# Kernel tuning notes

Hardware: AMD Instinct MI355X
Metric: run time of the kernel (lower is better)

Reference implementation:

```python
import jax, jax.numpy as jnp
import numpy as np

NUM_STEPS = 8
SLOPE = 25.0        # snntorch surrogate.fast_sigmoid default slope
MAX_STD = 2.0
MIN_STD = 0.1
STATE_DIM = 6
HIDDEN = 128
OUT = 1
BATCH = 65536
W_STD = 0.01


@jax.custom_vjp
def spike(x):
    # heaviside(x) with fast-sigmoid surrogate gradient
    return (x > 0).astype(x.dtype)

def _spike_fwd(x):
    return spike(x), x

def _spike_bwd(x, g):
    return (g / (SLOPE * jnp.abs(x) + 1.0) ** 2,)

spike.defvjp(_spike_fwd, _spike_bwd)


def setup_inputs() -> dict:
    key = jax.random.key(0)
    ks = jax.random.split(key, 8)
    state = jax.random.normal(ks[0], (BATCH, STATE_DIM), dtype=jnp.float32)
    w_fc1 = W_STD * jax.random.normal(ks[1], (HIDDEN, STATE_DIM), dtype=jnp.float32)
    w_rec1 = W_STD * jax.random.normal(ks[2], (HIDDEN, HIDDEN), dtype=jnp.float32)
    w_fc2 = W_STD * jax.random.normal(ks[3], (HIDDEN, HIDDEN), dtype=jnp.float32)
    w_rec2 = W_STD * jax.random.normal(ks[4], (HIDDEN, HIDDEN), dtype=jnp.float32)
    w_mean = W_STD * jax.random.normal(ks[5], (OUT, HIDDEN), dtype=jnp.float32)
    w_std = W_STD * jax.random.normal(ks[6], (OUT, HIDDEN), dtype=jnp.float32)
    return {
        "state": state,
        "w_fc1": w_fc1, "w_rec1": w_rec1,
        "w_fc2": w_fc2, "w_rec2": w_rec2,
        "w_mean": w_mean, "w_std": w_std,
        "alpha1": jnp.float32(0.9), "beta1": jnp.float32(0.9), "thr1": jnp.float32(1.0),
        "alpha2": jnp.float32(0.9), "beta2": jnp.float32(0.9), "thr2": jnp.float32(1.0),
    }


def _snn_forward(state, w_fc1, w_rec1, w_fc2, w_rec2, w_mean, w_std,
                 alpha1, beta1, thr1, alpha2, beta2, thr2):
    a1 = jnp.clip(alpha1, 0.0, 1.0); b1 = jnp.clip(beta1, 0.0, 1.0)
    a2 = jnp.clip(alpha2, 0.0, 1.0); b2 = jnp.clip(beta2, 0.0, 1.0)

    B = state.shape[0]
    cur1_in = state @ w_fc1.T  # constant across steps: [B, H]
    z = jnp.zeros((B, HIDDEN), dtype=state.dtype)

    def step(carry, _):
        syn1, mem1, spk1, syn2, mem2, spk2 = carry
        # layer 1: snntorch Synaptic (reset-by-subtract, reset from prev mem, detached)
        reset1 = jax.lax.stop_gradient((mem1 - thr1 > 0).astype(mem1.dtype))
        syn1 = a1 * syn1 + cur1_in + spk1 @ w_rec1.T
        mem1 = b1 * mem1 + syn1 - reset1 * thr1
        spk1 = spike(mem1 - thr1)
        # layer 2
        reset2 = jax.lax.stop_gradient((mem2 - thr2 > 0).astype(mem2.dtype))
        syn2 = a2 * syn2 + spk1 @ w_fc2.T + spk2 @ w_rec2.T
        mem2 = b2 * mem2 + syn2 - reset2 * thr2
        spk2 = spike(mem2 - thr2)
        return (syn1, mem1, spk1, syn2, mem2, spk2), spk2

    init = (z, z, z, z, z, z)
    _, spk_rec = jax.lax.scan(step, init, None, length=NUM_STEPS)  # [T, B, H]
    avg_spikes = spk_rec.mean(axis=0)  # [B, H]

    value_mean = jnp.tanh(avg_spikes @ w_mean.T)
    value_std = (MAX_STD - MIN_STD) * jax.nn.sigmoid(avg_spikes @ w_std.T + 2.0) + MIN_STD
    return value_mean, value_std


def reference(state, w_fc1, w_rec1, w_fc2, w_rec2, w_mean, w_std,
              alpha1, beta1, thr1, alpha2, beta2, thr2):
    return _snn_forward(state, w_fc1, w_rec1, w_fc2, w_rec2, w_mean, w_std,
                        alpha1, beta1, thr1, alpha2, beta2, thr2)
```

## Files before the change

kernel.cpp:

```cpp
#include <hip/hip_runtime.h>
#include <cmath>


constexpr int BATCH = 65536;
constexpr int HID   = 128;
constexpr int SDIM  = 6;
constexpr int NSTEP = 8;
constexpr int BLOCK = 1024;
constexpr int GRID  = 256;
constexpr int WAVES_TOTAL = GRID * (BLOCK / 64);
constexpr int ELEMS_PER_WAVE = BATCH / WAVES_TOTAL;

__global__ __launch_bounds__(BLOCK) void snn_fwd(
    const float* __restrict__ state,
    const float* __restrict__ w_fc1,
    const float* __restrict__ w_rec1,
    const float* __restrict__ w_fc2,
    const float* __restrict__ w_rec2,
    const float* __restrict__ w_mean,
    const float* __restrict__ w_std,
    const float* __restrict__ p_alpha1, const float* __restrict__ p_beta1,
    const float* __restrict__ p_thr1,
    const float* __restrict__ p_alpha2, const float* __restrict__ p_beta2,
    const float* __restrict__ p_thr2,
    float* __restrict__ out)
{
    __shared__ float2 ld_rec1[HID * 64];
    __shared__ float2 ld_fc2 [HID * 64];
    __shared__ float2 ld_fc1 [SDIM * 64];
    __shared__ float  ld_wm[HID];
    __shared__ float  ld_wsd[HID];

    const int tid = threadIdx.x;

    for (int v = tid; v < HID * 64; v += BLOCK) {
        const int l = v >> 7;
        const int j = v & 127;
        const int pos = (j << 6) | (l ^ (j & 63));
        ld_rec1[pos] = make_float2(w_rec1[l * HID + j], w_rec1[(l + 64) * HID + j]);
        ld_fc2 [pos] = make_float2(w_fc2 [l * HID + j], w_fc2 [(l + 64) * HID + j]);
    }
    for (int v = tid; v < SDIM * 64; v += BLOCK) {
        const int k = v >> 6, l = v & 63;
        ld_fc1[(k << 6) | l] = make_float2(w_fc1[l * SDIM + k], w_fc1[(l + 64) * SDIM + k]);
    }
    if (tid < HID)               ld_wm [tid]        = w_mean[tid];
    else if (tid < 2 * HID)      ld_wsd[tid - HID]  = w_std [tid - HID];

    const float a1 = fminf(fmaxf(p_alpha1[0], 0.f), 1.f);
    const float b1 = fminf(fmaxf(p_beta1 [0], 0.f), 1.f);
    const float a2 = fminf(fmaxf(p_alpha2[0], 0.f), 1.f);
    const float b2 = fminf(fmaxf(p_beta2 [0], 0.f), 1.f);
    const float t1 = p_thr1[0];
    const float t2 = p_thr2[0];

    __syncthreads();

    const int lane  = tid & 63;
    const int gwave = blockIdx.x * (BLOCK / 64) + (tid >> 6);

    for (int e = 0; e < ELEMS_PER_WAVE; ++e) {
        const int b = gwave + WAVES_TOTAL * e;

        float cur_a = 0.f, cur_b = 0.f;
        #pragma unroll
        for (int k = 0; k < SDIM; ++k) {
            const float s = state[b * SDIM + k];
            const float2 w = ld_fc1[(k << 6) | lane];
            cur_a = fmaf(s, w.x, cur_a);
            cur_b = fmaf(s, w.y, cur_b);
        }

        float syn1a = 0.f, syn1b = 0.f, mem1a = 0.f, mem1b = 0.f;
        float syn2a = 0.f, syn2b = 0.f, mem2a = 0.f, mem2b = 0.f;
        bool  spk1a = false, spk1b = false, spk2a = false, spk2b = false;
        float cnt_a = 0.f, cnt_b = 0.f;
        unsigned long long m1a = 0ull, m1b = 0ull, m2a = 0ull, m2b = 0ull;

        #pragma unroll 1
        for (int t = 0; t < NSTEP; ++t) {
            float r_a = 0.f, r_b = 0.f;
            unsigned long long m = m1a;
            while (m) {
                const int j = __builtin_ctzll(m); m &= m - 1;
                const float2 w = ld_rec1[(j << 6) | (lane ^ j)];
                r_a += w.x; r_b += w.y;
            }
            m = m1b;
            while (m) {
                const int j0 = __builtin_ctzll(m); m &= m - 1;
                const int j = j0 + 64;
                const float2 w = ld_rec1[(j << 6) | (lane ^ j0)];
                r_a += w.x; r_b += w.y;
            }
            syn1a = fmaf(a1, syn1a, cur_a + r_a);
            syn1b = fmaf(a1, syn1b, cur_b + r_b);
            mem1a = fmaf(b1, mem1a, syn1a) - (spk1a ? t1 : 0.f);
            mem1b = fmaf(b1, mem1b, syn1b) - (spk1b ? t1 : 0.f);
            spk1a = (mem1a - t1) > 0.f;
            spk1b = (mem1b - t1) > 0.f;
            m1a = __ballot(spk1a);
            m1b = __ballot(spk1b);

            float f_a = 0.f, f_b = 0.f;
            m = m1a;
            while (m) {
                const int j = __builtin_ctzll(m); m &= m - 1;
                const float2 w = ld_fc2[(j << 6) | (lane ^ j)];
                f_a += w.x; f_b += w.y;
            }
            m = m1b;
            while (m) {
                const int j0 = __builtin_ctzll(m); m &= m - 1;
                const int j = j0 + 64;
                const float2 w = ld_fc2[(j << 6) | (lane ^ j0)];
                f_a += w.x; f_b += w.y;
            }
            m = m2a;
            while (m) {
                const int j = __builtin_ctzll(m); m &= m - 1;
                f_a += w_rec2[lane * HID + j];
                f_b += w_rec2[(lane + 64) * HID + j];
            }
            m = m2b;
            while (m) {
                const int j = __builtin_ctzll(m) + 64; m &= m - 1;
                f_a += w_rec2[lane * HID + j];
                f_b += w_rec2[(lane + 64) * HID + j];
            }
            syn2a = fmaf(a2, syn2a, f_a);
            syn2b = fmaf(a2, syn2b, f_b);
            mem2a = fmaf(b2, mem2a, syn2a) - (spk2a ? t2 : 0.f);
            mem2b = fmaf(b2, mem2b, syn2b) - (spk2b ? t2 : 0.f);
            spk2a = (mem2a - t2) > 0.f;
            spk2b = (mem2b - t2) > 0.f;
            m2a = __ballot(spk2a);
            m2b = __ballot(spk2b);
            cnt_a += spk2a ? 1.f : 0.f;
            cnt_b += spk2b ? 1.f : 0.f;
        }

        const float avg_a = cnt_a * (1.f / (float)NSTEP);
        const float avg_b = cnt_b * (1.f / (float)NSTEP);
        float dm = avg_a * ld_wm [lane] + avg_b * ld_wm [lane + 64];
        float ds = avg_a * ld_wsd[lane] + avg_b * ld_wsd[lane + 64];
        #pragma unroll
        for (int off = 32; off > 0; off >>= 1) {
            dm += __shfl_xor(dm, off, 64);
            ds += __shfl_xor(ds, off, 64);
        }
        if (lane == 0) {
            out[b]         = tanhf(dm);
            const float sg = 1.f / (1.f + expf(-(ds + 2.f)));
            out[BATCH + b] = 1.9f * sg + 0.1f;
        }
    }
}

extern "C" void kernel_launch(void* const* d_in, const int* in_sizes, int n_in,
                              void* d_out, int out_size, void* d_ws, size_t ws_size,
                              hipStream_t stream) {
    (void)in_sizes; (void)n_in; (void)d_ws; (void)ws_size; (void)out_size;
    snn_fwd<<<GRID, BLOCK, 0, stream>>>(
        (const float*)d_in[0],
        (const float*)d_in[1],
        (const float*)d_in[2],
        (const float*)d_in[3],
        (const float*)d_in[4],
        (const float*)d_in[5],
        (const float*)d_in[6],
        (const float*)d_in[7],
        (const float*)d_in[8],
        (const float*)d_in[9],
        (const float*)d_in[10],
        (const float*)d_in[11],
        (const float*)d_in[12],
        (float*)d_out);
}
```

Measured before the change: 129.8 us.

## Fuse rec1/fc2 spike gathers into one float4 table and interleave two batch elements

Packs w_rec1 and w_fc2 columns into a single float4 shared-memory table, so one LDS read per active layer-1 spike serves both the next step's recurrent sum and the current fc2 sum. The recurrent layer-1 sum is deferred to the next step, so the two sparse loops over layer-1 spikes become one. Each wave now processes two batch elements at once inside a shared while-loop, to expose more independent loads and raise ILP. The cost is higher register pressure, a wider LDS access per iteration, and branch divergence when the two elements have different spike counts.

```diff
diff --git a/kernel.cpp b/kernel.cpp
--- a/kernel.cpp
+++ b/kernel.cpp
@@ -25,9 +25,8 @@
     const float* __restrict__ p_thr2,
     float* __restrict__ out)
 {
-    __shared__ float2 ld_rec1[HID * 64];
-    __shared__ float2 ld_fc2 [HID * 64];
-    __shared__ float2 ld_fc1 [SDIM * 64];
+    __shared__ float4 ld_w [HID * 64];
+    __shared__ float2 ld_fc1[SDIM * 64];
     __shared__ float  ld_wm[HID];
     __shared__ float  ld_wsd[HID];
 
@@ -37,15 +36,15 @@
         const int l = v >> 7;
         const int j = v & 127;
         const int pos = (j << 6) | (l ^ (j & 63));
-        ld_rec1[pos] = make_float2(w_rec1[l * HID + j], w_rec1[(l + 64) * HID + j]);
-        ld_fc2 [pos] = make_float2(w_fc2 [l * HID + j], w_fc2 [(l + 64) * HID + j]);
+        ld_w[pos] = make_float4(w_rec1[l * HID + j], w_rec1[(l + 64) * HID + j],
+                                w_fc2 [l * HID + j], w_fc2 [(l + 64) * HID + j]);
     }
     for (int v = tid; v < SDIM * 64; v += BLOCK) {
         const int k = v >> 6, l = v & 63;
         ld_fc1[(k << 6) | l] = make_float2(w_fc1[l * SDIM + k], w_fc1[(l + 64) * SDIM + k]);
     }
-    if (tid < HID)               ld_wm [tid]        = w_mean[tid];
-    else if (tid < 2 * HID)      ld_wsd[tid - HID]  = w_std [tid - HID];
+    if (tid < HID)               ld_wm [tid]       = w_mean[tid];
+    else if (tid < 2 * HID)      ld_wsd[tid - HID] = w_std [tid - HID];
 
     const float a1 = fminf(fmaxf(p_alpha1[0], 0.f), 1.f);
     const float b1 = fminf(fmaxf(p_beta1 [0], 0.f), 1.f);
@@ -59,100 +58,128 @@
     const int lane  = tid & 63;
     const int gwave = blockIdx.x * (BLOCK / 64) + (tid >> 6);
 
-    for (int e = 0; e < ELEMS_PER_WAVE; ++e) {
-        const int b = gwave + WAVES_TOTAL * e;
-
-        float cur_a = 0.f, cur_b = 0.f;
+    for (int e = 0; e < ELEMS_PER_WAVE / 2; ++e) {
+        int bidx[2];
+        bidx[0] = gwave + WAVES_TOTAL * (2 * e);
+        bidx[1] = gwave + WAVES_TOTAL * (2 * e + 1);
+
+        float cur_a[2], cur_b[2];
+        float s1a[2] = {0.f, 0.f}, s1b[2] = {0.f, 0.f};
+        float m1a[2] = {0.f, 0.f}, m1b[2] = {0.f, 0.f};
+        float s2a[2] = {0.f, 0.f}, s2b[2] = {0.f, 0.f};
+        float m2a[2] = {0.f, 0.f}, m2b[2] = {0.f, 0.f};
+        float ra [2] = {0.f, 0.f}, rb [2] = {0.f, 0.f};
+        float cna[2] = {0.f, 0.f}, cnb[2] = {0.f, 0.f};
+        bool sp1a[2] = {false, false}, sp1b[2] = {false, false};
+        bool sp2a[2] = {false, false}, sp2b[2] = {false, false};
+        unsigned long long M2a[2] = {0ull, 0ull}, M2b[2] = {0ull, 0ull};
+
         #pragma unroll
-        for (int k = 0; k < SDIM; ++k) {
-            const float s = state[b * SDIM + k];
-            const float2 w = ld_fc1[(k << 6) | lane];
-            cur_a = fmaf(s, w.x, cur_a);
-            cur_b = fmaf(s, w.y, cur_b);
-        }
-
-        float syn1a = 0.f, syn1b = 0.f, mem1a = 0.f, mem1b = 0.f;
-        float syn2a = 0.f, syn2b = 0.f, mem2a = 0.f, mem2b = 0.f;
-        bool  spk1a = false, spk1b = false, spk2a = false, spk2b = false;
-        float cnt_a = 0.f, cnt_b = 0.f;
-        unsigned long long m1a = 0ull, m1b = 0ull, m2a = 0ull, m2b = 0ull;
+        for (int p = 0; p < 2; ++p) {
+            float ca = 0.f, cb = 0.f;
+            #pragma unroll
+            for (int k = 0; k < SDIM; ++k) {
+                const float s = state[bidx[p] * SDIM + k];
+                const float2 w = ld_fc1[(k << 6) | lane];
+                ca = fmaf(s, w.x, ca);
+                cb = fmaf(s, w.y, cb);
+            }
+            cur_a[p] = ca; cur_b[p] = cb;
+        }
 
         #pragma unroll 1
         for (int t = 0; t < NSTEP; ++t) {
-            float r_a = 0.f, r_b = 0.f;
-            unsigned long long m = m1a;
-            while (m) {
-                const int j = __builtin_ctzll(m); m &= m - 1;
-                const float2 w = ld_rec1[(j << 6) | (lane ^ j)];
-                r_a += w.x; r_b += w.y;
-            }
-            m = m1b;
-            while (m) {
-                const int j0 = __builtin_ctzll(m); m &= m - 1;
-                const int j = j0 + 64;
-                const float2 w = ld_rec1[(j << 6) | (lane ^ j0)];
-                r_a += w.x; r_b += w.y;
-            }
-            syn1a = fmaf(a1, syn1a, cur_a + r_a);
-            syn1b = fmaf(a1, syn1b, cur_b + r_b);
-            mem1a = fmaf(b1, mem1a, syn1a) - (spk1a ? t1 : 0.f);
-            mem1b = fmaf(b1, mem1b, syn1b) - (spk1b ? t1 : 0.f);
-            spk1a = (mem1a - t1) > 0.f;
-            spk1b = (mem1b - t1) > 0.f;
-            m1a = __ballot(spk1a);
-            m1b = __ballot(spk1b);
-
-            float f_a = 0.f, f_b = 0.f;
-            m = m1a;
-            while (m) {
-                const int j = __builtin_ctzll(m); m &= m - 1;
-                const float2 w = ld_fc2[(j << 6) | (lane ^ j)];
-                f_a += w.x; f_b += w.y;
-            }
-            m = m1b;
-            while (m) {
-                const int j0 = __builtin_ctzll(m); m &= m - 1;
-                const int j = j0 + 64;
-                const float2 w = ld_fc2[(j << 6) | (lane ^ j0)];
-                f_a += w.x; f_b += w.y;
-            }
-            m = m2a;
-            while (m) {
-                const int j = __builtin_ctzll(m); m &= m - 1;
-                f_a += w_rec2[lane * HID + j];
-                f_b += w_rec2[(lane + 64) * HID + j];
-            }
-            m = m2b;
-            while (m) {
-                const int j = __builtin_ctzll(m) + 64; m &= m - 1;
-                f_a += w_rec2[lane * HID + j];
-                f_b += w_rec2[(lane + 64) * HID + j];
-            }
-            syn2a = fmaf(a2, syn2a, f_a);
-            syn2b = fmaf(a2, syn2b, f_b);
-            mem2a = fmaf(b2, mem2a, syn2a) - (spk2a ? t2 : 0.f);
-            mem2b = fmaf(b2, mem2b, syn2b) - (spk2b ? t2 : 0.f);
-            spk2a = (mem2a - t2) > 0.f;
-            spk2b = (mem2b - t2) > 0.f;
-            m2a = __ballot(spk2a);
-            m2b = __ballot(spk2b);
-            cnt_a += spk2a ? 1.f : 0.f;
-            cnt_b += spk2b ? 1.f : 0.f;
-        }
-
-        const float avg_a = cnt_a * (1.f / (float)NSTEP);
-        const float avg_b = cnt_b * (1.f / (float)NSTEP);
-        float dm = avg_a * ld_wm [lane] + avg_b * ld_wm [lane + 64];
-        float ds = avg_a * ld_wsd[lane] + avg_b * ld_wsd[lane + 64];
+            unsigned long long u0, v0, u1, v1;
+            #pragma unroll
+            for (int p = 0; p < 2; ++p) {
+                s1a[p] = fmaf(a1, s1a[p], cur_a[p] + ra[p]);
+                s1b[p] = fmaf(a1, s1b[p], cur_b[p] + rb[p]);
+                m1a[p] = fmaf(b1, m1a[p], s1a[p]) - (sp1a[p] ? t1 : 0.f);
+                m1b[p] = fmaf(b1, m1b[p], s1b[p]) - (sp1b[p] ? t1 : 0.f);
+                sp1a[p] = (m1a[p] - t1) > 0.f;
+                sp1b[p] = (m1b[p] - t1) > 0.f;
+                ra[p] = 0.f; rb[p] = 0.f;
+            }
+            u0 = __ballot(sp1a[0]); v0 = __ballot(sp1b[0]);
+            u1 = __ballot(sp1a[1]); v1 = __ballot(sp1b[1]);
+
+            float fa[2] = {0.f, 0.f}, fb[2] = {0.f, 0.f};
+            while (u0 | v0 | u1 | v1) {
+                if (u0) {
+                    const int j = __builtin_ctzll(u0); u0 &= u0 - 1;
+                    const float4 w = ld_w[(j << 6) | (lane ^ j)];
+                    ra[0] += w.x; rb[0] += w.y; fa[0] += w.z; fb[0] += w.w;
+                }
+                if (v0) {
+                    const int j0 = __builtin_ctzll(v0); v0 &= v0 - 1;
+                    const float4 w = ld_w[((j0 + 64) << 6) | (lane ^ j0)];
+                    ra[0] += w.x; rb[0] += w.y; fa[0] += w.z; fb[0] += w.w;
+                }
+                if (u1) {
+                    const int j = __builtin_ctzll(u1); u1 &= u1 - 1;
+                    const float4 w = ld_w[(j << 6) | (lane ^ j)];
+                    ra[1] += w.x; rb[1] += w.y; fa[1] += w.z; fb[1] += w.w;
+                }
+                if (v1) {
+                    const int j0 = __builtin_ctzll(v1); v1 &= v1 - 1;
+                    const float4 w = ld_w[((j0 + 64) << 6) | (lane ^ j0)];
+                    ra[1] += w.x; rb[1] += w.y; fa[1] += w.z; fb[1] += w.w;
+                }
+            }
+
+            #pragma unroll
+            for (int p = 0; p < 2; ++p) {
+                unsigned long long m = M2a[p];
+                while (m) {
+                    const int j = __builtin_ctzll(m); m &= m - 1;
+                    fa[p] += w_rec2[lane * HID + j];
+                    fb[p] += w_rec2[(lane + 64) * HID + j];
+                }
+                m = M2b[p];
+                while (m) {
+                    const int j = __builtin_ctzll(m) + 64; m &= m - 1;
+                    fa[p] += w_rec2[lane * HID + j];
+                    fb[p] += w_rec2[(lane + 64) * HID + j];
+                }
+            }
+
+            #pragma unroll
+            for (int p = 0; p < 2; ++p) {
+                s2a[p] = fmaf(a2, s2a[p], fa[p]);
+                s2b[p] = fmaf(a2, s2b[p], fb[p]);
+                m2a[p] = fmaf(b2, m2a[p], s2a[p]) - (sp2a[p] ? t2 : 0.f);
+                m2b[p] = fmaf(b2, m2b[p], s2b[p]) - (sp2b[p] ? t2 : 0.f);
+                sp2a[p] = (m2a[p] - t2) > 0.f;
+                sp2b[p] = (m2b[p] - t2) > 0.f;
+                cna[p] += sp2a[p] ? 1.f : 0.f;
+                cnb[p] += sp2b[p] ? 1.f : 0.f;
+            }
+            M2a[0] = __ballot(sp2a[0]); M2b[0] = __ballot(sp2b[0]);
+            M2a[1] = __ballot(sp2a[1]); M2b[1] = __ballot(sp2b[1]);
+        }
+
+        float dm[2], ds[2];
+        #pragma unroll
+        for (int p = 0; p < 2; ++p) {
+            const float avg_a = cna[p] * (1.f / (float)NSTEP);
+            const float avg_b = cnb[p] * (1.f / (float)NSTEP);
+            dm[p] = avg_a * ld_wm [lane] + avg_b * ld_wm [lane + 64];
+            ds[p] = avg_a * ld_wsd[lane] + avg_b * ld_wsd[lane + 64];
+        }
         #pragma unroll
         for (int off = 32; off > 0; off >>= 1) {
-            dm += __shfl_xor(dm, off, 64);
-            ds += __shfl_xor(ds, off, 64);
+            dm[0] += __shfl_xor(dm[0], off, 64);
+            ds[0] += __shfl_xor(ds[0], off, 64);
+            dm[1] += __shfl_xor(dm[1], off, 64);
+            ds[1] += __shfl_xor(ds[1], off, 64);
         }
         if (lane == 0) {
-            out[b]         = tanhf(dm);
-            const float sg = 1.f / (1.f + expf(-(ds + 2.f)));
-            out[BATCH + b] = 1.9f * sg + 0.1f;
+            #pragma unroll
+            for (int p = 0; p < 2; ++p) {
+                out[bidx[p]] = tanhf(dm[p]);
+                const float sg = 1.f / (1.f + expf(-(ds[p] + 2.f)));
+                out[BATCH + bidx[p]] = 1.9f * sg + 0.1f;
+            }
         }
     }
 }
```

Result: slower. 132.8 us (+2.3%).

## Split SNN forward into separate layer-1 and layer-2 kernels via spike-mask workspace

Applied to the files above, without the earlier changes.

Splits the fused two-layer recurrence into two kernels that communicate through per-element spike bitmasks written to the workspace. Each kernel stages only one 64KB weight matrix in LDS, which allows more blocks per CU, and the grid is doubled. Layer 2 skips leading timesteps with no layer-1 spikes and skips the output reduction when no layer-2 neuron fired. It also drops the XOR swizzle on LDS indexing. In exchange it adds a second launch and a global round trip for the masks, and the unswizzled layout may bring back LDS bank conflicts.

```diff
diff --git a/kernel.cpp b/kernel.cpp
--- a/kernel.cpp
+++ b/kernel.cpp
@@ -1,66 +1,48 @@
 #include <hip/hip_runtime.h>
 #include <cmath>
 
+
+typedef unsigned long long u64;
 
 constexpr int BATCH = 65536;
 constexpr int HID   = 128;
 constexpr int SDIM  = 6;
 constexpr int NSTEP = 8;
 constexpr int BLOCK = 1024;
-constexpr int GRID  = 256;
+constexpr int GRID  = 512;
 constexpr int WAVES_TOTAL = GRID * (BLOCK / 64);
-constexpr int ELEMS_PER_WAVE = BATCH / WAVES_TOTAL;
-
-__global__ __launch_bounds__(BLOCK) void snn_fwd(
+constexpr int EPW   = BATCH / WAVES_TOTAL;
+
+__global__ __launch_bounds__(BLOCK, 8) void snn_l1(
     const float* __restrict__ state,
     const float* __restrict__ w_fc1,
     const float* __restrict__ w_rec1,
-    const float* __restrict__ w_fc2,
-    const float* __restrict__ w_rec2,
-    const float* __restrict__ w_mean,
-    const float* __restrict__ w_std,
-    const float* __restrict__ p_alpha1, const float* __restrict__ p_beta1,
-    const float* __restrict__ p_thr1,
-    const float* __restrict__ p_alpha2, const float* __restrict__ p_beta2,
-    const float* __restrict__ p_thr2,
-    float* __restrict__ out)
+    const float* __restrict__ p_a1, const float* __restrict__ p_b1,
+    const float* __restrict__ p_t1,
+    u64* __restrict__ masks)
 {
-    __shared__ float2 ld_rec1[HID * 64];
-    __shared__ float2 ld_fc2 [HID * 64];
-    __shared__ float2 ld_fc1 [SDIM * 64];
-    __shared__ float  ld_wm[HID];
-    __shared__ float  ld_wsd[HID];
+    __shared__ float2 ld_r1 [HID * 64];
+    __shared__ float2 ld_fc1[SDIM * 64];
 
     const int tid = threadIdx.x;
-
     for (int v = tid; v < HID * 64; v += BLOCK) {
-        const int l = v >> 7;
-        const int j = v & 127;
-        const int pos = (j << 6) | (l ^ (j & 63));
-        ld_rec1[pos] = make_float2(w_rec1[l * HID + j], w_rec1[(l + 64) * HID + j]);
-        ld_fc2 [pos] = make_float2(w_fc2 [l * HID + j], w_fc2 [(l + 64) * HID + j]);
+        const int l = v & 63, j = v >> 6;
+        ld_r1[v] = make_float2(w_rec1[l * HID + j], w_rec1[(l + 64) * HID + j]);
     }
     for (int v = tid; v < SDIM * 64; v += BLOCK) {
-        const int k = v >> 6, l = v & 63;
-        ld_fc1[(k << 6) | l] = make_float2(w_fc1[l * SDIM + k], w_fc1[(l + 64) * SDIM + k]);
-    }
-    if (tid < HID)               ld_wm [tid]        = w_mean[tid];
-    else if (tid < 2 * HID)      ld_wsd[tid - HID]  = w_std [tid - HID];
-
-    const float a1 = fminf(fmaxf(p_alpha1[0], 0.f), 1.f);
-    const float b1 = fminf(fmaxf(p_beta1 [0], 0.f), 1.f);
-    const float a2 = fminf(fmaxf(p_alpha2[0], 0.f), 1.f);
-    const float b2 = fminf(fmaxf(p_beta2 [0], 0.f), 1.f);
-    const float t1 = p_thr1[0];
-    const float t2 = p_thr2[0];
-
+        const int l = v & 63, k = v >> 6;
+        ld_fc1[v] = make_float2(w_fc1[l * SDIM + k], w_fc1[(l + 64) * SDIM + k]);
+    }
+    const float a1 = fminf(fmaxf(p_a1[0], 0.f), 1.f);
+    const float b1 = fminf(fmaxf(p_b1[0], 0.f), 1.f);
+    const float t1 = p_t1[0];
     __syncthreads();
 
-    const int lane  = tid & 63;
-    const int gwave = blockIdx.x * (BLOCK / 64) + (tid >> 6);
-
-    for (int e = 0; e < ELEMS_PER_WAVE; ++e) {
-        const int b = gwave + WAVES_TOTAL * e;
+    const int lane = tid & 63;
+    const int gw   = blockIdx.x * (BLOCK / 64) + (tid >> 6);
+
+    for (int e = 0; e < EPW; ++e) {
+        const int b = gw + WAVES_TOTAL * e;
 
         float cur_a = 0.f, cur_b = 0.f;
         #pragma unroll
@@ -72,25 +54,23 @@
         }
 
         float syn1a = 0.f, syn1b = 0.f, mem1a = 0.f, mem1b = 0.f;
-        float syn2a = 0.f, syn2b = 0.f, mem2a = 0.f, mem2b = 0.f;
-        bool  spk1a = false, spk1b = false, spk2a = false, spk2b = false;
-        float cnt_a = 0.f, cnt_b = 0.f;
-        unsigned long long m1a = 0ull, m1b = 0ull, m2a = 0ull, m2b = 0ull;
+        bool  spk1a = false, spk1b = false;
+        u64   mu = 0ull, mv = 0ull;
+        u64* __restrict__ mp = masks + (size_t)b * (2 * NSTEP);
 
         #pragma unroll 1
         for (int t = 0; t < NSTEP; ++t) {
             float r_a = 0.f, r_b = 0.f;
-            unsigned long long m = m1a;
+            u64 m = mu;
             while (m) {
                 const int j = __builtin_ctzll(m); m &= m - 1;
-                const float2 w = ld_rec1[(j << 6) | (lane ^ j)];
+                const float2 w = ld_r1[(j << 6) | lane];
                 r_a += w.x; r_b += w.y;
             }
-            m = m1b;
-            while (m) {
-                const int j0 = __builtin_ctzll(m); m &= m - 1;
-                const int j = j0 + 64;
-                const float2 w = ld_rec1[(j << 6) | (lane ^ j0)];
+            m = mv;
+            while (m) {
+                const int j = __builtin_ctzll(m) + 64; m &= m - 1;
+                const float2 w = ld_r1[(j << 6) | lane];
                 r_a += w.x; r_b += w.y;
             }
             syn1a = fmaf(a1, syn1a, cur_a + r_a);
@@ -99,30 +79,81 @@
             mem1b = fmaf(b1, mem1b, syn1b) - (spk1b ? t1 : 0.f);
             spk1a = (mem1a - t1) > 0.f;
             spk1b = (mem1b - t1) > 0.f;
-            m1a = __ballot(spk1a);
-            m1b = __ballot(spk1b);
-
+            mu = __ballot(spk1a);
+            mv = __ballot(spk1b);
+            if (lane == 0) { mp[2 * t] = mu; mp[2 * t + 1] = mv; }
+        }
+    }
+}
+
+__global__ __launch_bounds__(BLOCK, 8) void snn_l2(
+    const float* __restrict__ w_fc2,
+    const float* __restrict__ w_rec2,
+    const float* __restrict__ w_mean,
+    const float* __restrict__ w_std,
+    const float* __restrict__ p_a2, const float* __restrict__ p_b2,
+    const float* __restrict__ p_t2,
+    const u64* __restrict__ masks,
+    float* __restrict__ out)
+{
+    __shared__ float2 ld_f2[HID * 64];
+    __shared__ float  ld_wm[HID];
+    __shared__ float  ld_wsd[HID];
+
+    const int tid = threadIdx.x;
+    for (int v = tid; v < HID * 64; v += BLOCK) {
+        const int l = v & 63, j = v >> 6;
+        ld_f2[v] = make_float2(w_fc2[l * HID + j], w_fc2[(l + 64) * HID + j]);
+    }
+    if (tid < HID)          ld_wm [tid]       = w_mean[tid];
+    else if (tid < 2 * HID) ld_wsd[tid - HID] = w_std [tid - HID];
+
+    const float a2 = fminf(fmaxf(p_a2[0], 0.f), 1.f);
+    const float b2 = fminf(fmaxf(p_b2[0], 0.f), 1.f);
+    const float t2 = p_t2[0];
+    __syncthreads();
+
+    const int lane = tid & 63;
+    const int gw   = blockIdx.x * (BLOCK / 64) + (tid >> 6);
+
+    for (int e = 0; e < EPW; ++e) {
+        const int b = gw + WAVES_TOTAL * e;
+
+        u64 mu[NSTEP], mv[NSTEP];
+        const u64* __restrict__ mp = masks + (size_t)b * (2 * NSTEP);
+        #pragma unroll
+        for (int t = 0; t < NSTEP; ++t) { mu[t] = mp[2 * t]; mv[t] = mp[2 * t + 1]; }
+
+        int t0 = 0;
+        while (t0 < NSTEP && (mu[t0] | mv[t0]) == 0ull) ++t0;
+
+        float syn2a = 0.f, syn2b = 0.f, mem2a = 0.f, mem2b = 0.f;
+        float cnt_a = 0.f, cnt_b = 0.f;
+        bool  spk2a = false, spk2b = false;
+        u64   Ma = 0ull, Mb = 0ull;
+
+        #pragma unroll 1
+        for (int t = t0; t < NSTEP; ++t) {
             float f_a = 0.f, f_b = 0.f;
-            m = m1a;
+            u64 m = mu[t];
             while (m) {
                 const int j = __builtin_ctzll(m); m &= m - 1;
-                const float2 w = ld_fc2[(j << 6) | (lane ^ j)];
+                const float2 w = ld_f2[(j << 6) | lane];
                 f_a += w.x; f_b += w.y;
             }
-            m = m1b;
-            while (m) {
-                const int j0 = __builtin_ctzll(m); m &= m - 1;
-                const int j = j0 + 64;
-                const float2 w = ld_fc2[(j << 6) | (lane ^ j0)];
+            m = mv[t];
+            while (m) {
+                const int j = __builtin_ctzll(m) + 64; m &= m - 1;
+                const float2 w = ld_f2[(j << 6) | lane];
                 f_a += w.x; f_b += w.y;
             }
-            m = m2a;
+            m = Ma;
             while (m) {
                 const int j = __builtin_ctzll(m); m &= m - 1;
                 f_a += w_rec2[lane * HID + j];
                 f_b += w_rec2[(lane + 64) * HID + j];
             }
-            m = m2b;
+            m = Mb;
             while (m) {
                 const int j = __builtin_ctzll(m) + 64; m &= m - 1;
                 f_a += w_rec2[lane * HID + j];
@@ -134,25 +165,34 @@
             mem2b = fmaf(b2, mem2b, syn2b) - (spk2b ? t2 : 0.f);
             spk2a = (mem2a - t2) > 0.f;
             spk2b = (mem2b - t2) > 0.f;
-            m2a = __ballot(spk2a);
-            m2b = __ballot(spk2b);
+            Ma = __ballot(spk2a);
+            Mb = __ballot(spk2b);
             cnt_a += spk2a ? 1.f : 0.f;
             cnt_b += spk2b ? 1.f : 0.f;
         }
 
-        const float avg_a = cnt_a * (1.f / (float)NSTEP);
-        const float avg_b = cnt_b * (1.f / (float)NSTEP);
-        float dm = avg_a * ld_wm [lane] + avg_b * ld_wm [lane + 64];
-        float ds = avg_a * ld_wsd[lane] + avg_b * ld_wsd[lane + 64];
-        #pragma unroll
-        for (int off = 32; off > 0; off >>= 1) {
-            dm += __shfl_xor(dm, off, 64);
-            ds += __shfl_xor(ds, off, 64);
-        }
-        if (lane == 0) {
-            out[b]         = tanhf(dm);
-            const float sg = 1.f / (1.f + expf(-(ds + 2.f)));
-            out[BATCH + b] = 1.9f * sg + 0.1f;
+        const bool any = (cnt_a != 0.f) || (cnt_b != 0.f);
+        if (__ballot(any) == 0ull) {
+            if (lane == 0) {
+                out[b] = 0.f;
+                const float sg = 1.f / (1.f + expf(-2.0f));
+                out[BATCH + b] = 1.9f * sg + 0.1f;
+            }
+        } else {
+            const float avg_a = cnt_a * 0.125f;
+            const float avg_b = cnt_b * 0.125f;
+            float dm = avg_a * ld_wm [lane] + avg_b * ld_wm [lane + 64];
+            float ds = avg_a * ld_wsd[lane] + avg_b * ld_wsd[lane + 64];
+            #pragma unroll
+            for (int off = 32; off > 0; off >>= 1) {
+                dm += __shfl_xor(dm, off, 64);
+                ds += __shfl_xor(ds, off, 64);
+            }
+            if (lane == 0) {
+                out[b] = tanhf(dm);
+                const float sg = 1.f / (1.f + expf(-(ds + 2.f)));
+                out[BATCH + b] = 1.9f * sg + 0.1f;
+            }
         }
     }
 }
@@ -160,20 +200,24 @@
 extern "C" void kernel_launch(void* const* d_in, const int* in_sizes, int n_in,
                               void* d_out, int out_size, void* d_ws, size_t ws_size,
                               hipStream_t stream) {
-    (void)in_sizes; (void)n_in; (void)d_ws; (void)ws_size; (void)out_size;
-    snn_fwd<<<GRID, BLOCK, 0, stream>>>(
+    (void)in_sizes; (void)n_in; (void)out_size; (void)ws_size;
+    u64* masks = (u64*)d_ws;
+    snn_l1<<<GRID, BLOCK, 0, stream>>>(
         (const float*)d_in[0],
         (const float*)d_in[1],
         (const float*)d_in[2],
+        (const float*)d_in[7],
+        (const float*)d_in[8],
+        (const float*)d_in[9],
+        masks);
+    snn_l2<<<GRID, BLOCK, 0, stream>>>(
         (const float*)d_in[3],
         (const float*)d_in[4],
         (const float*)d_in[5],
         (const float*)d_in[6],
-        (const float*)d_in[7],
-        (const float*)d_in[8],
-        (const float*)d_in[9],
         (const float*)d_in[10],
         (const float*)d_in[11],
         (const float*)d_in[12],
+        masks,
         (float*)d_out);
 }
```

New measurement: 162.5 us. +25.2%, slower.

## Fuse rec1 and fc2 spike gathers into one interleaved LDS pass

Applied to the files above, without the earlier changes.

Interleaves the w_rec1 and w_fc2 columns into one float4 LDS table so each spiking layer-1 neuron drives a single 128-bit read that feeds both the next step's recurrent input and the current fc2 input. The recurrent contribution is carried across steps instead of being recomputed from the previous mask, which removes one full pass over the spike bitmask per step. The spike loop is also unrolled by two to overlap LDS loads. The XOR swizzle is dropped in favour of a lane-contiguous layout, and the carried rr from the final step is computed but never used.

```diff
diff --git a/kernel.cpp b/kernel.cpp
--- a/kernel.cpp
+++ b/kernel.cpp
@@ -1,6 +1,10 @@
 #include <hip/hip_runtime.h>
 #include <cmath>
 
+
+typedef float v2f __attribute__((ext_vector_type(2)));
+typedef float v4f __attribute__((ext_vector_type(4)));
+typedef unsigned long long u64;
 
 constexpr int BATCH = 65536;
 constexpr int HID   = 128;
@@ -9,7 +13,7 @@
 constexpr int BLOCK = 1024;
 constexpr int GRID  = 256;
 constexpr int WAVES_TOTAL = GRID * (BLOCK / 64);
-constexpr int ELEMS_PER_WAVE = BATCH / WAVES_TOTAL;
+constexpr int EPW   = BATCH / WAVES_TOTAL;
 
 __global__ __launch_bounds__(BLOCK) void snn_fwd(
     const float* __restrict__ state,
@@ -19,48 +23,45 @@
     const float* __restrict__ w_rec2,
     const float* __restrict__ w_mean,
     const float* __restrict__ w_std,
-    const float* __restrict__ p_alpha1, const float* __restrict__ p_beta1,
-    const float* __restrict__ p_thr1,
-    const float* __restrict__ p_alpha2, const float* __restrict__ p_beta2,
-    const float* __restrict__ p_thr2,
+    const float* __restrict__ p_a1, const float* __restrict__ p_b1,
+    const float* __restrict__ p_t1,
+    const float* __restrict__ p_a2, const float* __restrict__ p_b2,
+    const float* __restrict__ p_t2,
     float* __restrict__ out)
 {
-    __shared__ float2 ld_rec1[HID * 64];
-    __shared__ float2 ld_fc2 [HID * 64];
-    __shared__ float2 ld_fc1 [SDIM * 64];
-    __shared__ float  ld_wm[HID];
-    __shared__ float  ld_wsd[HID];
+    __shared__ v4f   ld_w [HID * 64];
+    __shared__ float2 ld_fc1[SDIM * 64];
+    __shared__ float ld_wm[HID];
+    __shared__ float ld_wsd[HID];
 
     const int tid = threadIdx.x;
 
     for (int v = tid; v < HID * 64; v += BLOCK) {
-        const int l = v >> 7;
-        const int j = v & 127;
-        const int pos = (j << 6) | (l ^ (j & 63));
-        ld_rec1[pos] = make_float2(w_rec1[l * HID + j], w_rec1[(l + 64) * HID + j]);
-        ld_fc2 [pos] = make_float2(w_fc2 [l * HID + j], w_fc2 [(l + 64) * HID + j]);
+        const int l = v & 63, j = v >> 6;
+        ld_w[v] = (v4f){ w_rec1[l * HID + j], w_rec1[(l + 64) * HID + j],
+                         w_fc2 [l * HID + j], w_fc2 [(l + 64) * HID + j] };
     }
     for (int v = tid; v < SDIM * 64; v += BLOCK) {
-        const int k = v >> 6, l = v & 63;
-        ld_fc1[(k << 6) | l] = make_float2(w_fc1[l * SDIM + k], w_fc1[(l + 64) * SDIM + k]);
+        const int l = v & 63, k = v >> 6;
+        ld_fc1[v] = make_float2(w_fc1[l * SDIM + k], w_fc1[(l + 64) * SDIM + k]);
     }
-    if (tid < HID)               ld_wm [tid]        = w_mean[tid];
-    else if (tid < 2 * HID)      ld_wsd[tid - HID]  = w_std [tid - HID];
+    if (tid < HID)          ld_wm [tid]       = w_mean[tid];
+    else if (tid < 2 * HID) ld_wsd[tid - HID] = w_std [tid - HID];
 
-    const float a1 = fminf(fmaxf(p_alpha1[0], 0.f), 1.f);
-    const float b1 = fminf(fmaxf(p_beta1 [0], 0.f), 1.f);
-    const float a2 = fminf(fmaxf(p_alpha2[0], 0.f), 1.f);
-    const float b2 = fminf(fmaxf(p_beta2 [0], 0.f), 1.f);
-    const float t1 = p_thr1[0];
-    const float t2 = p_thr2[0];
+    const float a1 = fminf(fmaxf(p_a1[0], 0.f), 1.f);
+    const float b1 = fminf(fmaxf(p_b1[0], 0.f), 1.f);
+    const float a2 = fminf(fmaxf(p_a2[0], 0.f), 1.f);
+    const float b2 = fminf(fmaxf(p_b2[0], 0.f), 1.f);
+    const float t1 = p_t1[0];
+    const float t2 = p_t2[0];
 
     __syncthreads();
 
-    const int lane  = tid & 63;
-    const int gwave = blockIdx.x * (BLOCK / 64) + (tid >> 6);
+    const int lane = tid & 63;
+    const int gw   = blockIdx.x * (BLOCK / 64) + (tid >> 6);
 
-    for (int e = 0; e < ELEMS_PER_WAVE; ++e) {
-        const int b = gwave + WAVES_TOTAL * e;
+    for (int e = 0; e < EPW; ++e) {
+        const int b = gw + WAVES_TOTAL * e;
 
         float cur_a = 0.f, cur_b = 0.f;
         #pragma unroll
@@ -75,47 +76,52 @@
         float syn2a = 0.f, syn2b = 0.f, mem2a = 0.f, mem2b = 0.f;
         bool  spk1a = false, spk1b = false, spk2a = false, spk2b = false;
         float cnt_a = 0.f, cnt_b = 0.f;
-        unsigned long long m1a = 0ull, m1b = 0ull, m2a = 0ull, m2b = 0ull;
+        u64   m2a = 0ull, m2b = 0ull;
+        v2f   rr = {0.f, 0.f};
 
         #pragma unroll 1
         for (int t = 0; t < NSTEP; ++t) {
-            float r_a = 0.f, r_b = 0.f;
-            unsigned long long m = m1a;
-            while (m) {
-                const int j = __builtin_ctzll(m); m &= m - 1;
-                const float2 w = ld_rec1[(j << 6) | (lane ^ j)];
-                r_a += w.x; r_b += w.y;
-            }
-            m = m1b;
-            while (m) {
-                const int j0 = __builtin_ctzll(m); m &= m - 1;
-                const int j = j0 + 64;
-                const float2 w = ld_rec1[(j << 6) | (lane ^ j0)];
-                r_a += w.x; r_b += w.y;
-            }
-            syn1a = fmaf(a1, syn1a, cur_a + r_a);
-            syn1b = fmaf(a1, syn1b, cur_b + r_b);
+            syn1a = fmaf(a1, syn1a, cur_a + rr.x);
+            syn1b = fmaf(a1, syn1b, cur_b + rr.y);
             mem1a = fmaf(b1, mem1a, syn1a) - (spk1a ? t1 : 0.f);
             mem1b = fmaf(b1, mem1b, syn1b) - (spk1b ? t1 : 0.f);
             spk1a = (mem1a - t1) > 0.f;
             spk1b = (mem1b - t1) > 0.f;
-            m1a = __ballot(spk1a);
-            m1b = __ballot(spk1b);
+            const u64 mu = __ballot(spk1a);
+            const u64 mv = __ballot(spk1b);
 
-            float f_a = 0.f, f_b = 0.f;
-            m = m1a;
-            while (m) {
-                const int j = __builtin_ctzll(m); m &= m - 1;
-                const float2 w = ld_fc2[(j << 6) | (lane ^ j)];
-                f_a += w.x; f_b += w.y;
-            }
-            m = m1b;
+            rr = (v2f){0.f, 0.f};
+            v2f ff = {0.f, 0.f};
+            u64 m = mu;
             while (m) {
                 const int j0 = __builtin_ctzll(m); m &= m - 1;
-                const int j = j0 + 64;
-                const float2 w = ld_fc2[(j << 6) | (lane ^ j0)];
-                f_a += w.x; f_b += w.y;
+                if (m) {
+                    const int j1 = __builtin_ctzll(m); m &= m - 1;
+                    const v4f w0 = ld_w[(j0 << 6) | lane];
+                    const v4f w1 = ld_w[(j1 << 6) | lane];
+                    rr += w0.lo; ff += w0.hi;
+                    rr += w1.lo; ff += w1.hi;
+                } else {
+                    const v4f w0 = ld_w[(j0 << 6) | lane];
+                    rr += w0.lo; ff += w0.hi;
+                }
             }
+            m = mv;
+            while (m) {
+                const int j0 = __builtin_ctzll(m) + 64; m &= m - 1;
+                if (m) {
+                    const int j1 = __builtin_ctzll(m) + 64; m &= m - 1;
+                    const v4f w0 = ld_w[(j0 << 6) | lane];
+                    const v4f w1 = ld_w[(j1 << 6) | lane];
+                    rr += w0.lo; ff += w0.hi;
+                    rr += w1.lo; ff += w1.hi;
+                } else {
+                    const v4f w0 = ld_w[(j0 << 6) | lane];
+                    rr += w0.lo; ff += w0.hi;
+                }
+            }
+
+            float f_a = ff.x, f_b = ff.y;
             m = m2a;
             while (m) {
                 const int j = __builtin_ctzll(m); m &= m - 1;
@@ -128,6 +134,7 @@
                 f_a += w_rec2[lane * HID + j];
                 f_b += w_rec2[(lane + 64) * HID + j];
             }
+
             syn2a = fmaf(a2, syn2a, f_a);
             syn2b = fmaf(a2, syn2b, f_b);
             mem2a = fmaf(b2, mem2a, syn2a) - (spk2a ? t2 : 0.f);
@@ -140,8 +147,8 @@
             cnt_b += spk2b ? 1.f : 0.f;
         }
 
-        const float avg_a = cnt_a * (1.f / (float)NSTEP);
-        const float avg_b = cnt_b * (1.f / (float)NSTEP);
+        const float avg_a = cnt_a * 0.125f;
+        const float avg_b = cnt_b * 0.125f;
         float dm = avg_a * ld_wm [lane] + avg_b * ld_wm [lane + 64];
         float ds = avg_a * ld_wsd[lane] + avg_b * ld_wsd[lane + 64];
         #pragma unroll
@@ -150,7 +157,7 @@
             ds += __shfl_xor(ds, off, 64);
         }
         if (lane == 0) {
-            out[b]         = tanhf(dm);
+            out[b] = tanhf(dm);
             const float sg = 1.f / (1.f + expf(-(ds + 2.f)));
             out[BATCH + b] = 1.9f * sg + 0.1f;
         }
```

Result: slower. 141.2 us (+8.8%).
